# Optimization experiments

Measured on AMD Instinct MI355X. Metric: run time of the kernel, lower is better.

Reference implementation:

```python
import jax, jax.numpy as jnp
import numpy as np

ED = 200      # entity/relation dim
KW = 9        # kernel width
OC = 32       # out channels
WOUT = ED - KW + 1  # 192 valid-conv output width
B = 1024
NE = 40943
NR = 18


def setup_inputs() -> dict:
    key = jax.random.key(0)
    ks = jax.random.split(key, 9)
    g = lambda k, shape: jax.random.normal(k, shape, jnp.float32) * 0.05
    return dict(
        e1_idx=jax.random.randint(ks[0], (B,), 0, NE, dtype=jnp.int32),
        r_idx=jax.random.randint(ks[1], (B,), 0, NR, dtype=jnp.int32),
        W1=g(ks[2], (ED, KW * OC)),
        b1=g(ks[3], (KW * OC,)),
        W2=g(ks[4], (WOUT * OC, ED)),
        b2=g(ks[5], (ED,)),
        bias_logits=g(ks[6], (NE,)),
        E=g(ks[7], (NE, ED)),
        R=g(ks[8], (NR, ED)),
    )


def reference(e1_idx, r_idx, W1, b1, W2, b2, bias_logits, E, R):
    e1 = E[e1_idx]          # [B, 200]
    r = R[r_idx]            # [B, 200]
    # hypernetwork: relation -> per-sample conv filters [B, KW, OC]
    k = (r @ W1 + b1).reshape(-1, KW, OC)
    # per-sample valid 1D conv of e1 with its own filters (depthwise-as-groups trick collapsed)
    idx = jnp.arange(WOUT)[:, None] + jnp.arange(KW)[None, :]  # [WOUT, KW]
    patches = e1[:, idx]                                        # [B, WOUT, KW]
    # flatten order matches TF: (out_channel major, width minor)
    feat = jnp.einsum('bwj,bjo->bow', patches, k).reshape(e1.shape[0], OC * WOUT)
    h = jax.nn.relu(feat @ W2 + b2)                             # [B, 200]
    logits = h @ E.T + bias_logits                              # [B, NE]
    return logits
```

## Files before the change

### kernel.cpp

```cpp
#include <hip/hip_runtime.h>

#define NE 40943
#define NR 18
#define ED 200
#define KWC 9
#define OC 32
#define WOUT 192
#define KOC 288
#define KH 224

typedef unsigned short u16;
typedef unsigned int u32;
typedef __bf16 bf16x8 __attribute__((ext_vector_type(8)));
typedef float f32x4 __attribute__((ext_vector_type(4)));
typedef u16 u16x8 __attribute__((ext_vector_type(8)));
typedef u16 u16x4 __attribute__((ext_vector_type(4)));

__device__ __forceinline__ u16 f2bf(float f) {
  u32 u = __builtin_bit_cast(u32, f);
  u32 r = (u + 0x7fffu + ((u >> 16) & 1u)) >> 16;
  return (u16)r;
}

__device__ __forceinline__ void gl_lds16(const u16* g, u16* l) {
  __builtin_amdgcn_global_load_lds(
      (const __attribute__((address_space(1))) u32*)g,
      (__attribute__((address_space(3))) u32*)l, 16, 0, 0);
}

__global__ void prep_k_kernel(const float* __restrict__ R,
                              const float* __restrict__ W1,
                              const float* __restrict__ b1,
                              float* __restrict__ KrT) {
  int rel = blockIdx.x;
  int j = threadIdx.x;
  float acc = b1[j];
  const float* rrow = R + rel * ED;
  for (int d = 0; d < ED; ++d) acc += rrow[d] * W1[d * KOC + j];
  KrT[j * NR + rel] = acc;
}

__global__ __launch_bounds__(256) void build_c_kernel(const float* __restrict__ KrT,
                                                      const float* __restrict__ W2,
                                                      float* __restrict__ C) {
  int p = blockIdx.x;
  int d = threadIdx.x;
  int jlo = p > (WOUT - 1) ? p - (WOUT - 1) : 0;
  int jhi = p < (KWC - 1) ? p : (KWC - 1);
  if (d < ED) {
    float acc[NR];
#pragma unroll
    for (int r = 0; r < NR; ++r) acc[r] = 0.f;
    for (int j = jlo; j <= jhi; ++j) {
      int w = p - j;
      const float* w2base = W2 + (size_t)w * ED + d;
      const float* kb = KrT + (j * OC) * NR;
#pragma unroll
      for (int o = 0; o < OC; ++o) {
        float w2v = w2base[(size_t)o * WOUT * ED];
#pragma unroll
        for (int r = 0; r < NR; ++r) acc[r] += kb[o * NR + r] * w2v;
      }
    }
#pragma unroll
    for (int r = 0; r < NR; ++r) C[((size_t)r * ED + p) * ED + d] = acc[r];
  }
}

__global__ __launch_bounds__(256) void h_kernel(const int* __restrict__ e1_idx,
                                                const int* __restrict__ r_idx,
                                                const float* __restrict__ E,
                                                const float* __restrict__ C,
                                                const float* __restrict__ b2,
                                                u16* __restrict__ Hb) {
  __shared__ float e1s[ED];
  int b = blockIdx.x;
  int t = threadIdx.x;
  if (t < ED) e1s[t] = E[(size_t)e1_idx[b] * ED + t];
  __syncthreads();
  int r = r_idx[b];
  const float* Cr = C + (size_t)r * ED * ED;
  if (t < KH) {
    float acc = 0.f;
    if (t < ED) {
#pragma unroll 8
      for (int p = 0; p < ED; ++p) acc += e1s[p] * Cr[(size_t)p * ED + t];
      acc += b2[t];
      acc = acc > 0.f ? acc : 0.f;
    }
    Hb[(size_t)b * KH + t] = (t < ED) ? f2bf(acc) : (u16)0;
  }
}

__global__ void conv_e_kernel(const float* __restrict__ E, u16* __restrict__ Eb) {
  int idx = blockIdx.x * 256 + threadIdx.x;
  const int total = NE * (KH / 4);
  if (idx >= total) return;
  int row = idx / (KH / 4);
  int c4 = (idx % (KH / 4)) * 4;
  u16x4 st = {0, 0, 0, 0};
  if (c4 < ED) {
    f32x4 v = *(const f32x4*)(E + (size_t)row * ED + c4);
    st[0] = f2bf(v[0]); st[1] = f2bf(v[1]); st[2] = f2bf(v[2]); st[3] = f2bf(v[3]);
  }
  *(u16x4*)(Eb + (size_t)row * KH + c4) = st;
}

__global__ __launch_bounds__(256) void gemm2_kernel(
    const u16* __restrict__ Hb,
    const u16* __restrict__ Eb,
    const float* __restrict__ bias,
    float* __restrict__ out) {
  __shared__ __align__(16) u16 lA[2][128 * 32];
  __shared__ __align__(16) u16 lB[2][128 * 32];
  const int t = threadIdx.x;
  const int wave = t >> 6, lane = t & 63;

  int id = blockIdx.x;
  int xcd = id & 7;
  int q = id >> 3;
  int bx = xcd * 40 + q % 40;
  int by = q / 40;
  const int m0 = by * 128;
  const int n0 = bx * 128;
  const int wm = (wave >> 1) * 64, wn = (wave & 1) * 64;
  const int lr = lane & 15, lq = lane >> 4;
  const int csw = (lq ^ ((lr >> 1) & 3)) * 8;

  int aoff[2], boff[2], loff[2];
#pragma unroll
  for (int s = 0; s < 2; ++s) {
    int chunk = wave * 128 + s * 64 + lane;
    int r = chunk >> 2, cc = chunk & 3;
    int ccs = cc ^ ((r >> 1) & 3);
    loff[s] = chunk * 8;
    aoff[s] = (m0 + r) * KH + ccs * 8;
    int gr = n0 + r;
    if (gr > NE - 1) gr = NE - 1;
    boff[s] = gr * KH + ccs * 8;
  }

  f32x4 zero = {0.f, 0.f, 0.f, 0.f};
  f32x4 acc[4][4];
#pragma unroll
  for (int i = 0; i < 4; ++i)
#pragma unroll
    for (int j = 0; j < 4; ++j) acc[i][j] = zero;

#pragma unroll
  for (int s = 0; s < 2; ++s) {
    gl_lds16(Hb + aoff[s], &lA[0][loff[s]]);
    gl_lds16(Eb + boff[s], &lB[0][loff[s]]);
  }
  __syncthreads();

  int cur = 0;
  for (int kt = 0; kt < KH / 32; ++kt) {
    if (kt < KH / 32 - 1) {
      int k0 = (kt + 1) * 32;
#pragma unroll
      for (int s = 0; s < 2; ++s) {
        gl_lds16(Hb + aoff[s] + k0, &lA[cur ^ 1][loff[s]]);
        gl_lds16(Eb + boff[s] + k0, &lB[cur ^ 1][loff[s]]);
      }
    }
    bf16x8 af[4], bfv[4];
#pragma unroll
    for (int mi = 0; mi < 4; ++mi) {
      int rr = wm + mi * 16 + lr;
      af[mi] = *(const bf16x8*)(&lA[cur][rr * 32 + csw]);
    }
#pragma unroll
    for (int ni = 0; ni < 4; ++ni) {
      int rr = wn + ni * 16 + lr;
      bfv[ni] = *(const bf16x8*)(&lB[cur][rr * 32 + csw]);
    }
#pragma unroll
    for (int mi = 0; mi < 4; ++mi)
#pragma unroll
      for (int ni = 0; ni < 4; ++ni)
        acc[mi][ni] = __builtin_amdgcn_mfma_f32_16x16x32_bf16(af[mi], bfv[ni], acc[mi][ni], 0, 0, 0);
    __syncthreads();
    cur ^= 1;
  }

#pragma unroll
  for (int mi = 0; mi < 4; ++mi) {
    int row = m0 + wm + mi * 16 + lq * 4;
#pragma unroll
    for (int ni = 0; ni < 4; ++ni) {
      int col = n0 + wn + ni * 16 + lr;
      if (col < NE) {
        float bv = bias[col];
#pragma unroll
        for (int i = 0; i < 4; ++i)
          out[(size_t)(row + i) * NE + col] = acc[mi][ni][i] + bv;
      }
    }
  }
}

extern "C" void kernel_launch(void* const* d_in, const int* in_sizes, int n_in,
                              void* d_out, int out_size, void* d_ws, size_t ws_size,
                              hipStream_t stream) {
  const int* e1_idx = (const int*)d_in[0];
  const int* r_idx = (const int*)d_in[1];
  const float* W1 = (const float*)d_in[2];
  const float* b1 = (const float*)d_in[3];
  const float* W2 = (const float*)d_in[4];
  const float* b2 = (const float*)d_in[5];
  const float* bias_logits = (const float*)d_in[6];
  const float* E = (const float*)d_in[7];
  const float* R = (const float*)d_in[8];
  float* out = (float*)d_out;

  char* ws = (char*)d_ws;
  float* KrT = (float*)ws;
  float* C = (float*)(ws + 32768);
  u16* Hb = (u16*)(ws + 32768 + 2880000);
  u16* Eb = (u16*)(ws + 32768 + 2880000 + 458752);

  prep_k_kernel<<<dim3(NR), dim3(KOC), 0, stream>>>(R, W1, b1, KrT);
  build_c_kernel<<<dim3(ED), dim3(256), 0, stream>>>(KrT, W2, C);
  h_kernel<<<dim3(1024), dim3(256), 0, stream>>>(e1_idx, r_idx, E, C, b2, Hb);
  conv_e_kernel<<<dim3((NE * (KH / 4) + 255) / 256), dim3(256), 0, stream>>>(E, Eb);
  gemm2_kernel<<<dim3(320 * 8), dim3(256), 0, stream>>>(Hb, Eb, bias_logits, out);
}
```

Before: 309.5 us.

## Triple-buffer GEMM K-loop with explicit vmcnt waits and full unroll

Replaces the double-buffered LDS pipeline in the logits GEMM with a three-stage ring. Global-to-LDS loads are issued two tiles ahead, and the seven K iterations are fully unrolled with explicit s_waitcnt vmcnt counts and raw s_barrier calls. MFMA blocks are wrapped in s_setprio raises. The goal is to hide global load latency better and cut barrier overhead, at the cost of 50% more LDS per block, which may reduce occupancy.

```diff
diff --git a/kernel.cpp b/kernel.cpp
--- a/kernel.cpp
+++ b/kernel.cpp
@@ -111,8 +111,8 @@
     const u16* __restrict__ Eb,
     const float* __restrict__ bias,
     float* __restrict__ out) {
-  __shared__ __align__(16) u16 lA[2][128 * 32];
-  __shared__ __align__(16) u16 lB[2][128 * 32];
+  __shared__ __align__(16) u16 lA[3][128 * 32];
+  __shared__ __align__(16) u16 lB[3][128 * 32];
   const int t = threadIdx.x;
   const int wave = t >> 6, lane = t & 63;
 
@@ -147,42 +147,58 @@
 #pragma unroll
     for (int j = 0; j < 4; ++j) acc[i][j] = zero;
 
-#pragma unroll
-  for (int s = 0; s < 2; ++s) {
-    gl_lds16(Hb + aoff[s], &lA[0][loff[s]]);
-    gl_lds16(Eb + boff[s], &lB[0][loff[s]]);
-  }
-  __syncthreads();
-
-  int cur = 0;
-  for (int kt = 0; kt < KH / 32; ++kt) {
-    if (kt < KH / 32 - 1) {
-      int k0 = (kt + 1) * 32;
-#pragma unroll
-      for (int s = 0; s < 2; ++s) {
-        gl_lds16(Hb + aoff[s] + k0, &lA[cur ^ 1][loff[s]]);
-        gl_lds16(Eb + boff[s] + k0, &lB[cur ^ 1][loff[s]]);
-      }
-    }
-    bf16x8 af[4], bfv[4];
-#pragma unroll
-    for (int mi = 0; mi < 4; ++mi) {
-      int rr = wm + mi * 16 + lr;
-      af[mi] = *(const bf16x8*)(&lA[cur][rr * 32 + csw]);
-    }
-#pragma unroll
-    for (int ni = 0; ni < 4; ++ni) {
-      int rr = wn + ni * 16 + lr;
-      bfv[ni] = *(const bf16x8*)(&lB[cur][rr * 32 + csw]);
-    }
-#pragma unroll
-    for (int mi = 0; mi < 4; ++mi)
-#pragma unroll
-      for (int ni = 0; ni < 4; ++ni)
-        acc[mi][ni] = __builtin_amdgcn_mfma_f32_16x16x32_bf16(af[mi], bfv[ni], acc[mi][ni], 0, 0, 0);
-    __syncthreads();
-    cur ^= 1;
-  }
+#define GSTAGE(kt, c)                                      \
+  do {                                                     \
+    gl_lds16(Hb + aoff[0] + (kt) * 32, &lA[c][loff[0]]);   \
+    gl_lds16(Eb + boff[0] + (kt) * 32, &lB[c][loff[0]]);   \
+    gl_lds16(Hb + aoff[1] + (kt) * 32, &lA[c][loff[1]]);   \
+    gl_lds16(Eb + boff[1] + (kt) * 32, &lB[c][loff[1]]);   \
+  } while (0)
+
+#define WAIT_SB(n)                                         \
+  do {                                                     \
+    asm volatile("s_waitcnt vmcnt(" #n ")" ::: "memory");  \
+    __builtin_amdgcn_sched_barrier(0);                     \
+    __builtin_amdgcn_s_barrier();                          \
+    __builtin_amdgcn_sched_barrier(0);                     \
+  } while (0)
+
+#define KITER(kt, cur, dostage)                                                   \
+  do {                                                                            \
+    bf16x8 af[4], bfv[4];                                                         \
+    _Pragma("unroll") for (int mi = 0; mi < 4; ++mi)                              \
+        af[mi] = *(const bf16x8*)(&lA[cur][(wm + mi * 16 + lr) * 32 + csw]);      \
+    _Pragma("unroll") for (int ni = 0; ni < 4; ++ni)                              \
+        bfv[ni] = *(const bf16x8*)(&lB[cur][(wn + ni * 16 + lr) * 32 + csw]);     \
+    asm volatile("s_waitcnt lgkmcnt(0)" ::: "memory");                            \
+    __builtin_amdgcn_sched_barrier(0);                                            \
+    __builtin_amdgcn_s_barrier();                                                 \
+    __builtin_amdgcn_sched_barrier(0);                                            \
+    if (dostage) GSTAGE((kt) + 3, cur);                                           \
+    __builtin_amdgcn_s_setprio(1);                                                \
+    _Pragma("unroll") for (int mi = 0; mi < 4; ++mi)                              \
+        _Pragma("unroll") for (int ni = 0; ni < 4; ++ni)                          \
+            acc[mi][ni] = __builtin_amdgcn_mfma_f32_16x16x32_bf16(                \
+                af[mi], bfv[ni], acc[mi][ni], 0, 0, 0);                           \
+    __builtin_amdgcn_s_setprio(0);                                                \
+  } while (0)
+
+  GSTAGE(0, 0);
+  GSTAGE(1, 1);
+  GSTAGE(2, 2);
+  WAIT_SB(8);
+
+  KITER(0, 0, 1); WAIT_SB(8);
+  KITER(1, 1, 1); WAIT_SB(8);
+  KITER(2, 2, 1); WAIT_SB(8);
+  KITER(3, 0, 1); WAIT_SB(8);
+  KITER(4, 1, 0); WAIT_SB(4);
+  KITER(5, 2, 0); WAIT_SB(0);
+  KITER(6, 0, 0);
+
+#undef KITER
+#undef WAIT_SB
+#undef GSTAGE
 
 #pragma unroll
   for (int mi = 0; mi < 4; ++mi) {
```

Result: faster. 303.1 us (-2.1%).
